# Kernel tuning notes

Measured on AMD Instinct MI355X. Metric: run time of the kernel, lower is better.

## Reference

```python
import jax, jax.numpy as jnp
import numpy as np

B, S, E, H = 4, 2048, 1024, 16
D = E // H  # head dim = 64


def setup_inputs() -> dict:
    key = jax.random.key(0)
    ks = jax.random.split(key, 5)
    s = 0.02
    return {
        "x": jax.random.normal(ks[0], (B, S, E), dtype=jnp.float32),
        "Wq": jax.random.normal(ks[1], (E, E), dtype=jnp.float32) * s,
        "Wk": jax.random.normal(ks[2], (E, E), dtype=jnp.float32) * s,
        "Wv": jax.random.normal(ks[3], (E, E), dtype=jnp.float32) * s,
        "Wo": jax.random.normal(ks[4], (E, E), dtype=jnp.float32) * s,
        "bo": jnp.zeros((E,), dtype=jnp.float32),
    }


def reference(x, Wq, Wk, Wv, Wo, bo):
    b, s, e = x.shape
    h, d = H, e // H
    # QKV projections -> [b, h, s, d]
    q = (x @ Wq).reshape(b, s, h, d).transpose(0, 2, 1, 3)
    k = (x @ Wk).reshape(b, s, h, d).transpose(0, 2, 1, 3)
    v = (x @ Wv).reshape(b, s, h, d).transpose(0, 2, 1, 3)
    # scores [b, h, s, s], causal mask with -inf, scaled softmax
    a = jnp.einsum('bhqd,bhkd->bhqk', q, k)
    causal = jnp.tril(jnp.ones((s, s), dtype=bool))  # True where allowed
    a = jnp.where(causal, a, -jnp.inf) / jnp.sqrt(jnp.asarray(d, x.dtype))
    a = jax.nn.softmax(a, axis=-1)
    # dropout p=0.0 (identity in eval)
    y = jnp.einsum('bhqk,bhkd->bhqd', a, v)
    y = y.transpose(0, 2, 1, 3).reshape(b, s, e)
    return y @ Wo + bo
```

## Files before the change

### kernel.cpp

```cpp
#include <hip/hip_runtime.h>

typedef __bf16 bf16x8 __attribute__((ext_vector_type(8)));
typedef float f32x4 __attribute__((ext_vector_type(4)));
typedef float f32x16 __attribute__((ext_vector_type(16)));
typedef unsigned short u16x8 __attribute__((ext_vector_type(8)));
typedef unsigned int u32x4 __attribute__((ext_vector_type(4)));
typedef unsigned int u32x2v __attribute__((ext_vector_type(2)));

#define S_LEN 2048
#define NHEAD 16
#define HDIM  64
#define EMB   1024

__device__ __forceinline__ ushort f2b(float v) {
  union { float f; unsigned u; } x; x.f = v;
  unsigned r = (x.u + 0x7fffu + ((x.u >> 16) & 1u)) >> 16;
  return (ushort)r;
}

__device__ __forceinline__ unsigned pk2(float lo, float hi) {
  union { float f; unsigned u; } a, b; a.f = lo; b.f = hi;
  return (b.u & 0xffff0000u) | (a.u >> 16);
}

typedef const __attribute__((address_space(1))) unsigned int* gp1_t;
typedef __attribute__((address_space(3))) unsigned int* lp3_t;
__device__ __forceinline__ void gld16(const ushort* g, const ushort* l) {
  __builtin_amdgcn_global_load_lds((gp1_t)(unsigned long long)(uintptr_t)g,
                                   (lp3_t)(unsigned int)(uintptr_t)l, 16, 0, 0);
}

__device__ __forceinline__ void barf() {
  asm volatile("" ::: "memory");
  __builtin_amdgcn_s_barrier();
  asm volatile("" ::: "memory");
}

__global__ __launch_bounds__(256) void prep_kernel(
    const float* __restrict__ x, const float* __restrict__ W0,
    const float* __restrict__ W1, const float* __restrict__ W2,
    const float* __restrict__ W3, ushort* __restrict__ xb,
    ushort* __restrict__ Wt0, ushort* __restrict__ Wt1,
    ushort* __restrict__ Wt2, ushort* __restrict__ Wt3, float scale0) {
  const int z = blockIdx.z;
  if (z == 4) {
    size_t base = ((size_t)(blockIdx.y * 32 + blockIdx.x)) * 8192 + threadIdx.x * 4;
#pragma unroll
    for (int i = 0; i < 8; ++i) {
      float4 v = *(const float4*)(x + base + i * 1024);
      ushort4 o;
      o.x = f2b(v.x); o.y = f2b(v.y); o.z = f2b(v.z); o.w = f2b(v.w);
      *(ushort4*)(xb + base + i * 1024) = o;
    }
    return;
  }
  __shared__ float t[32][33];
  const float* W = z == 0 ? W0 : (z == 1 ? W1 : (z == 2 ? W2 : W3));
  ushort* Wt = z == 0 ? Wt0 : (z == 1 ? Wt1 : (z == 2 ? Wt2 : Wt3));
  const float scale = z == 0 ? scale0 : 1.0f;
  int k0 = blockIdx.x * 32, n0 = blockIdx.y * 32;
  int c = threadIdx.x & 31, r0 = threadIdx.x >> 5;
#pragma unroll
  for (int i = 0; i < 4; ++i) {
    int r = r0 + i * 8;
    t[r][c] = W[(size_t)(k0 + r) * EMB + n0 + c];
  }
  __syncthreads();
#pragma unroll
  for (int i = 0; i < 4; ++i) {
    int r = r0 + i * 8;
    Wt[(size_t)(n0 + r) * EMB + k0 + c] = f2b(t[c][r] * scale);
  }
}

template <int EPI>
__global__ __launch_bounds__(512, 2) void gemm8_kernel(
    const ushort* __restrict__ A, const ushort* __restrict__ Bt,
    ushort* __restrict__ outQ, ushort* __restrict__ outK, ushort* __restrict__ outVt,
    float* __restrict__ outF, const float* __restrict__ bias) {
  __shared__ ushort lds8[73728];
  const int tid = threadIdx.x;
  const int wave = tid >> 6, lane = tid & 63, ln = lane & 15, quad = lane >> 4;
  const int wm = wave >> 2, wn = wave & 3;
  const long m0 = (long)blockIdx.x * 128, n0 = (long)blockIdx.y * 256;
  constexpr int K = EMB, KT = K / 64;

  const int srow = tid >> 3;
  const int scol = ((tid & 7) ^ (srow & 7)) * 8;
  const ushort* srcA = A + (m0 + srow) * (long)K + scol;
  const ushort* srcB = Bt + (n0 + srow) * (long)K + scol;

#define STG_A(t, s)                                                            \
  do {                                                                         \
    gld16(srcA + (t) * 64,               lds8 + (s) * 8192 + tid * 8);         \
    gld16(srcA + (t) * 64 + 64 * K,      lds8 + (s) * 8192 + 4096 + tid * 8);  \
  } while (0)
#define STG_B(t, s)                                                            \
  do {                                                                         \
    gld16(srcB + (t) * 64,               lds8 + 24576 + (s) * 16384 + tid * 8);         \
    gld16(srcB + (t) * 64 + 64 * K,      lds8 + 24576 + (s) * 16384 + 4096 + tid * 8);  \
    gld16(srcB + (t) * 64 + 128 * K,     lds8 + 24576 + (s) * 16384 + 8192 + tid * 8);  \
    gld16(srcB + (t) * 64 + 192 * K,     lds8 + 24576 + (s) * 16384 + 12288 + tid * 8); \
  } while (0)

  const int sw = (ln & 7) * 8;

#define RD_A(F, kk, s)                                                         \
  do {                                                                         \
    const ushort* p_ = lds8 + (s) * 8192 + (wm * 64 + ln) * 64 +               \
                       (((kk) * 32 + quad * 8) ^ sw);                          \
    F[0] = *(const bf16x8*)p_;                                                 \
    F[1] = *(const bf16x8*)(p_ + 1024);                                        \
    F[2] = *(const bf16x8*)(p_ + 2048);                                        \
    F[3] = *(const bf16x8*)(p_ + 3072);                                        \
  } while (0)
#define RD_B(F, kk, s)                                                         \
  do {                                                                         \
    const ushort* p_ = lds8 + 24576 + (s) * 16384 + (wn * 64 + ln) * 64 +      \
                       (((kk) * 32 + quad * 8) ^ sw);                          \
    F[0] = *(const bf16x8*)p_;                                                 \
    F[1] = *(const bf16x8*)(p_ + 1024);                                        \
    F[2] = *(const bf16x8*)(p_ + 2048);                                        \
    F[3] = *(const bf16x8*)(p_ + 3072);                                        \
  } while (0)

#define MM16(AF, BF)                                                           \
  do {                                                                         \
    __builtin_amdgcn_s_setprio(1);                                             \
    _Pragma("unroll") for (int mt = 0; mt < 4; ++mt)                           \
        _Pragma("unroll") for (int nt = 0; nt < 4; ++nt)                       \
            acc[mt][nt] = __builtin_amdgcn_mfma_f32_16x16x32_bf16(             \
                AF[mt], BF[nt], acc[mt][nt], 0, 0, 0);                         \
    __builtin_amdgcn_s_setprio(0);                                             \
  } while (0)

  f32x4 acc[4][4] = {};
  bf16x8 afP[4], bfP[4], afN[4], bfN[4];

  STG_A(0, 0); STG_B(0, 0);
  STG_A(1, 1); STG_B(1, 1);
  asm volatile("s_waitcnt vmcnt(6)" ::: "memory");
  barf();
  RD_A(afP, 0, 0); RD_B(bfP, 0, 0);

#define TILE_FULL(t, s, s1, s2)                                                \
  do {                                                                         \
    STG_A((t) + 2, s2);                                                        \
    RD_A(afN, 1, s); RD_B(bfN, 1, s);                                          \
    MM16(afP, bfP);                                                            \
    STG_B((t) + 2, s2);                                                        \
    asm volatile("s_waitcnt vmcnt(6) lgkmcnt(0)" ::: "memory");                \
    barf();                                                                    \
    RD_A(afP, 0, s1); RD_B(bfP, 0, s1);                                        \
    MM16(afN, bfN);                                                            \
  } while (0)

  for (int th = 0; th < 12; th += 3) {
    TILE_FULL(th, 0, 1, 2);
    TILE_FULL(th + 1, 1, 2, 0);
    TILE_FULL(th + 2, 2, 0, 1);
  }
  TILE_FULL(12, 0, 1, 2);
  TILE_FULL(13, 1, 2, 0);
  RD_A(afN, 1, 2); RD_B(bfN, 1, 2);
  MM16(afP, bfP);
  asm volatile("s_waitcnt vmcnt(0) lgkmcnt(0)" ::: "memory");
  barf();
  RD_A(afP, 0, 0); RD_B(bfP, 0, 0);
  MM16(afN, bfN);
  RD_A(afN, 1, 0); RD_B(bfN, 1, 0);
  MM16(afP, bfP);
  MM16(afN, bfN);

  if (EPI == 0) {
    const int sel = (int)(n0 >> 10);
    if (sel == 2) {
#pragma unroll
      for (int mt = 0; mt < 4; ++mt) {
        const long mbase = m0 + wm * 64 + mt * 16 + quad * 4;
        const long bb = mbase >> 11, s = mbase & 2047;
#pragma unroll
        for (int nt = 0; nt < 4; ++nt) {
          const int nn = (int)((n0 & 1023) + wn * 64 + nt * 16 + ln);
          const int h = nn >> 6, d = nn & 63;
          uint2 val;
          val.x = (unsigned)f2b(acc[mt][nt][0]) | ((unsigned)f2b(acc[mt][nt][1]) << 16);
          val.y = (unsigned)f2b(acc[mt][nt][2]) | ((unsigned)f2b(acc[mt][nt][3]) << 16);
          *(uint2*)(outVt + (((bb * NHEAD + h) * (long)HDIM + d) * S_LEN) + s) = val;
        }
      }
    } else {
      ushort* dst = sel == 0 ? outQ : outK;
#pragma unroll
      for (int mt = 0; mt < 4; ++mt) {
#pragma unroll
        for (int nt = 0; nt < 4; ++nt) {
          const int nn = (int)((n0 & 1023) + wn * 64 + nt * 16 + ln);
          const int h = nn >> 6, d = nn & 63;
#pragma unroll
          for (int r = 0; r < 4; ++r) {
            const long m = m0 + wm * 64 + mt * 16 + quad * 4 + r;
            const long bb = m >> 11, s = m & 2047;
            dst[(((bb * NHEAD + h) * S_LEN) + s) * HDIM + d] = f2b(acc[mt][nt][r]);
          }
        }
      }
    }
  } else {
#pragma unroll
    for (int mt = 0; mt < 4; ++mt) {
#pragma unroll
      for (int nt = 0; nt < 4; ++nt) {
        const long n = n0 + wn * 64 + nt * 16 + ln;
        const float bv = bias[n];
#pragma unroll
        for (int r = 0; r < 4; ++r) {
          const long m = m0 + wm * 64 + mt * 16 + quad * 4 + r;
          outF[m * (long)EMB + n] = acc[mt][nt][r] + bv;
        }
      }
    }
  }
#undef TILE_FULL
#undef MM16
#undef RD_B
#undef RD_A
#undef STG_B
#undef STG_A
}

__global__ __launch_bounds__(256, 3) void attn_kernel(const ushort* __restrict__ Q,
                                                      const ushort* __restrict__ Kg,
                                                      const ushort* __restrict__ Vt,
                                                      ushort* __restrict__ Y) {
  __shared__ alignas(16) ushort Ks[3][4096];
  __shared__ alignas(16) ushort Vs[3][4096];
  const int tid = threadIdx.x;
  const int wave = tid >> 6, lane = tid & 63;
  const int l31 = lane & 31, hi = lane >> 5;
  const int bh = blockIdx.x;
  const int qb = 15 - (int)blockIdx.y;
  const int q0 = qb * 128;
  const size_t base = (size_t)bh * S_LEN * HDIM;
  const int ntiles = 2 * qb + 2;

  const u16x8 ob = {0x3F80, 0x3F80, 0x3F80, 0x3F80, 0x3F80, 0x3F80, 0x3F80, 0x3F80};
  const bf16x8 ones = __builtin_bit_cast(bf16x8, ob);

  bf16x8 qf[4];
#pragma unroll
  for (int dsub = 0; dsub < 4; ++dsub)
    qf[dsub] = *(const bf16x8*)(Q + base + (size_t)(q0 + wave * 32 + l31) * HDIM +
                                dsub * 16 + hi * 8);

  f32x16 acc0 = {}, acc1 = {}, accl = {};

  const int srow = tid >> 3;
  const int scc  = ((tid & 7) ^ (srow & 7)) * 8;
  const ushort* KgS = Kg + base + (size_t)srow * HDIM + scc;
  const ushort* VgS = Vt + base + (size_t)srow * S_LEN + scc;

#define STAGE(t, s)                                                            \
  do {                                                                         \
    const size_t kk_ = (size_t)(t) * 64;                                       \
    gld16(KgS + kk_ * HDIM,               &Ks[s][0] + tid * 8);                \
    gld16(KgS + (kk_ + 32) * HDIM,        &Ks[s][0] + 2048 + tid * 8);         \
    gld16(VgS + kk_,                      &Vs[s][0] + tid * 8);                \
    gld16(VgS + 32 * (size_t)S_LEN + kk_, &Vs[s][0] + 2048 + tid * 8);         \
  } while (0)

  STAGE(0, 0);
  STAGE(1, 1);
  asm volatile("s_waitcnt vmcnt(4)" ::: "memory");
  barf();

  const int swL = (lane & 7) * 8;
  const int qbase = q0 + wave * 32;
  int sc = 0, sn = 1, ss = 2;

  for (int kt = 0; kt < ntiles; ++kt) {
    const int k0 = kt * 64;
    const bool do_stage = (kt + 2 < ntiles);
    if (do_stage) STAGE(kt + 2, ss);

    const ushort* Kc = &Ks[sc][0];
    const ushort* Vc = &Vs[sc][0];

    if (k0 < qbase + 32) {
      f32x16 sT0 = {}, sT1 = {};
      __builtin_amdgcn_s_setprio(1);
#pragma unroll
      for (int dsub = 0; dsub < 4; ++dsub) {
        const int c = (dsub * 16 + hi * 8) ^ swL;
        bf16x8 kf0 = *(const bf16x8*)(Kc + l31 * 64 + c);
        bf16x8 kf1 = *(const bf16x8*)(Kc + (32 + l31) * 64 + c);
        sT0 = __builtin_amdgcn_mfma_f32_32x32x16_bf16(kf0, qf[dsub], sT0, 0, 0, 0);
        sT1 = __builtin_amdgcn_mfma_f32_32x32x16_bf16(kf1, qf[dsub], sT1, 0, 0, 0);
      }
      __builtin_amdgcn_s_setprio(0);

      if (k0 + 63 > qbase) {
        const int rowq = qbase + l31;
#pragma unroll
        for (int r = 0; r < 16; ++r) {
          const int key = k0 + ((r & 3) + 8 * (r >> 2)) + 4 * hi;
          if (key > rowq) sT0[r] = -3.0e38f;
          if (key + 32 > rowq) sT1[r] = -3.0e38f;
        }
      }

      unsigned pw0[8], pw1[8];
#pragma unroll
      for (int i = 0; i < 8; ++i) {
        pw0[i] = pk2(__builtin_amdgcn_exp2f(sT0[2 * i]),
                     __builtin_amdgcn_exp2f(sT0[2 * i + 1]));
        pw1[i] = pk2(__builtin_amdgcn_exp2f(sT1[2 * i]),
                     __builtin_amdgcn_exp2f(sT1[2 * i + 1]));
      }

#define KEYBLK(PW, KSQ0)                                                       \
  do {                                                                         \
    u32x2v r02 = __builtin_amdgcn_permlane32_swap(PW[0], PW[2], false, false); \
    u32x2v r13 = __builtin_amdgcn_permlane32_swap(PW[1], PW[3], false, false); \
    u32x2v r46 = __builtin_amdgcn_permlane32_swap(PW[4], PW[6], false, false); \
    u32x2v r57 = __builtin_amdgcn_permlane32_swap(PW[5], PW[7], false, false); \
    u32x4 fwA, fwB;                                                            \
    fwA[0] = r02[0]; fwA[1] = r13[0]; fwA[2] = r02[1]; fwA[3] = r13[1];        \
    fwB[0] = r46[0]; fwB[1] = r57[0]; fwB[2] = r46[1]; fwB[3] = r57[1];        \
    bf16x8 paA = __builtin_bit_cast(bf16x8, fwA);                              \
    bf16x8 paB = __builtin_bit_cast(bf16x8, fwB);                              \
    __builtin_amdgcn_s_setprio(1);                                             \
    accl = __builtin_amdgcn_mfma_f32_32x32x16_bf16(paA, ones, accl, 0, 0, 0);  \
    accl = __builtin_amdgcn_mfma_f32_32x32x16_bf16(paB, ones, accl, 0, 0, 0);  \
    {                                                                          \
      const int vcA = (((KSQ0)) * 16 + hi * 8) ^ swL;                          \
      bf16x8 va0 = *(const bf16x8*)(Vc + l31 * 64 + vcA);                      \
      bf16x8 va1 = *(const bf16x8*)(Vc + (32 + l31) * 64 + vcA);               \
      acc0 = __builtin_amdgcn_mfma_f32_32x32x16_bf16(paA, va0, acc0, 0, 0, 0); \
      acc1 = __builtin_amdgcn_mfma_f32_32x32x16_bf16(paA, va1, acc1, 0, 0, 0); \
      const int vcB = (((KSQ0) + 1) * 16 + hi * 8) ^ swL;                      \
      bf16x8 vb0 = *(const bf16x8*)(Vc + l31 * 64 + vcB);                      \
      bf16x8 vb1 = *(const bf16x8*)(Vc + (32 + l31) * 64 + vcB);               \
      acc0 = __builtin_amdgcn_mfma_f32_32x32x16_bf16(paB, vb0, acc0, 0, 0, 0); \
      acc1 = __builtin_amdgcn_mfma_f32_32x32x16_bf16(paB, vb1, acc1, 0, 0, 0); \
    }                                                                          \
    __builtin_amdgcn_s_setprio(0);                                             \
  } while (0)

      KEYBLK(pw0, 0);
      KEYBLK(pw1, 2);
#undef KEYBLK
    }

    if (kt + 1 < ntiles) {
      if (do_stage) {
        asm volatile("s_waitcnt vmcnt(4) lgkmcnt(0)" ::: "memory");
      } else {
        asm volatile("s_waitcnt vmcnt(0) lgkmcnt(0)" ::: "memory");
      }
      barf();
    }
    const int t_ = sc; sc = sn; sn = ss; ss = t_;
  }
#undef STAGE

  const long b = bh >> 4;
  const int h = bh & 15;
#pragma unroll
  for (int r = 0; r < 16; ++r) {
    const float inv = 1.0f / accl[r];
    const int qq = q0 + wave * 32 + ((r & 3) + 8 * (r >> 2)) + 4 * hi;
    ushort* yp = Y + (((b * S_LEN + qq) * NHEAD) + h) * HDIM;
    yp[l31]      = f2b(acc0[r] * inv);
    yp[32 + l31] = f2b(acc1[r] * inv);
  }
}

extern "C" void kernel_launch(void* const* d_in, const int* in_sizes, int n_in,
                              void* d_out, int out_size, void* d_ws, size_t ws_size,
                              hipStream_t stream) {
  const float* x  = (const float*)d_in[0];
  const float* Wq = (const float*)d_in[1];
  const float* Wk = (const float*)d_in[2];
  const float* Wv = (const float*)d_in[3];
  const float* Wo = (const float*)d_in[4];
  const float* bo = (const float*)d_in[5];
  float* out = (float*)d_out;

  const size_t XE = (size_t)8192 * EMB;
  ushort* ws    = (ushort*)d_ws;
  ushort* xb    = ws;
  ushort* Wtqkv = xb + XE;
  ushort* Wto   = Wtqkv + 3 * 1048576;
  ushort* Qb    = Wto + 1048576;
  ushort* Kb    = Qb + XE;
  ushort* Vtb   = Kb + XE;
  ushort* Yb    = xb;

  const float SCALE_Q = 1.4426950408889634f / 8.0f;

  prep_kernel<<<dim3(32, 32, 5), 256, 0, stream>>>(
      x, Wq, Wk, Wv, Wo, xb, Wtqkv, Wtqkv + 1048576, Wtqkv + 2097152, Wto, SCALE_Q);

  gemm8_kernel<0><<<dim3(64, 12), 512, 0, stream>>>(xb, Wtqkv, Qb, Kb, Vtb,
                                                    nullptr, nullptr);
  attn_kernel<<<dim3(64, 16), 256, 0, stream>>>(Qb, Kb, Vtb, Yb);
  gemm8_kernel<1><<<dim3(64, 4), 512, 0, stream>>>(Yb, Wto, nullptr, nullptr,
                                                   nullptr, out, bo);
}
```

Before: 229.7 us.

## Use 256x256 tile GEMM kernel with double buffering for QKV projection

Adds a dedicated QKV projection kernel with 256x256 output tiles, where each wave computes a 128x64 subtile (8x4 MFMAs) from a two-stage LDS double buffer. The old 128x256 triple-buffered path is kept only for the output projection. Larger tiles raise arithmetic intensity and cut global reloads of A and B. In exchange the grid shrinks to 384 blocks, which may underfill the GPU. The kernel also uses more accumulator registers and 128KB of LDS, which can limit occupancy and latency hiding.

```diff
diff --git a/kernel.cpp b/kernel.cpp
--- a/kernel.cpp
+++ b/kernel.cpp
@@ -73,10 +73,125 @@
   }
 }
 
+__global__ __launch_bounds__(512, 2) void gemm256_kernel(
+    const ushort* __restrict__ A, const ushort* __restrict__ Bt,
+    ushort* __restrict__ outQ, ushort* __restrict__ outK,
+    ushort* __restrict__ outVt) {
+  __shared__ ushort lds2[65536];
+  const int tid = threadIdx.x;
+  const int wave = tid >> 6, lane = tid & 63, ln = lane & 15, quad = lane >> 4;
+  const int wm = wave >> 2, wn = wave & 3;
+  const long m0 = (long)blockIdx.x * 256, n0 = (long)blockIdx.y * 256;
+  constexpr int K = EMB, KT = K / 64;
+
+  const int srow = tid >> 3;
+  const int scol = ((tid & 7) ^ (srow & 7)) * 8;
+  const ushort* srcA = A + (m0 + srow) * (long)K + scol;
+  const ushort* srcB = Bt + (n0 + srow) * (long)K + scol;
+
+#define STG_A(t, b)                                                            \
+  do {                                                                         \
+    _Pragma("unroll") for (int ld = 0; ld < 4; ++ld)                           \
+        gld16(srcA + (t) * 64 + ld * 64 * K,                                   \
+              lds2 + (b) * 16384 + ld * 4096 + tid * 8);                       \
+  } while (0)
+#define STG_B(t, b)                                                            \
+  do {                                                                         \
+    _Pragma("unroll") for (int ld = 0; ld < 4; ++ld)                           \
+        gld16(srcB + (t) * 64 + ld * 64 * K,                                   \
+              lds2 + 32768 + (b) * 16384 + ld * 4096 + tid * 8);               \
+  } while (0)
+
+  const int sw = (ln & 7) * 8;
+
+#define RD_A8(F, kk, b)                                                        \
+  do {                                                                         \
+    const ushort* p_ = lds2 + (b) * 16384 + (wm * 128 + ln) * 64 +             \
+                       (((kk) * 32 + quad * 8) ^ sw);                          \
+    _Pragma("unroll") for (int m_ = 0; m_ < 8; ++m_)                           \
+        F[m_] = *(const bf16x8*)(p_ + m_ * 1024);                              \
+  } while (0)
+#define RD_B4(F, kk, b)                                                        \
+  do {                                                                         \
+    const ushort* p_ = lds2 + 32768 + (b) * 16384 + (wn * 64 + ln) * 64 +      \
+                       (((kk) * 32 + quad * 8) ^ sw);                          \
+    _Pragma("unroll") for (int n_ = 0; n_ < 4; ++n_)                           \
+        F[n_] = *(const bf16x8*)(p_ + n_ * 1024);                              \
+  } while (0)
+
+#define MM32(AF, BF)                                                           \
+  do {                                                                         \
+    __builtin_amdgcn_s_setprio(1);                                             \
+    _Pragma("unroll") for (int mt = 0; mt < 8; ++mt)                           \
+        _Pragma("unroll") for (int nt = 0; nt < 4; ++nt)                       \
+            acc[mt][nt] = __builtin_amdgcn_mfma_f32_16x16x32_bf16(             \
+                AF[mt], BF[nt], acc[mt][nt], 0, 0, 0);                         \
+    __builtin_amdgcn_s_setprio(0);                                             \
+  } while (0)
+
+  f32x4 acc[8][4] = {};
+  bf16x8 afP[8], bfP[4], afN[8], bfN[4];
+
+  STG_A(0, 0); STG_B(0, 0);
+  asm volatile("s_waitcnt vmcnt(0)" ::: "memory");
+  barf();
+
+  for (int kt = 0; kt < KT; ++kt) {
+    const int bb = kt & 1;
+    if (kt + 1 < KT) { STG_A(kt + 1, bb ^ 1); STG_B(kt + 1, bb ^ 1); }
+    RD_A8(afP, 0, bb); RD_B4(bfP, 0, bb);
+    MM32(afP, bfP);
+    RD_A8(afN, 1, bb); RD_B4(bfN, 1, bb);
+    MM32(afN, bfN);
+    if (kt + 1 < KT) {
+      asm volatile("s_waitcnt vmcnt(0) lgkmcnt(0)" ::: "memory");
+      barf();
+    }
+  }
+
+  const int sel = (int)(n0 >> 10);
+  if (sel == 2) {
+#pragma unroll
+    for (int mt = 0; mt < 8; ++mt) {
+      const long mbase = m0 + wm * 128 + mt * 16 + quad * 4;
+      const long bb2 = mbase >> 11, s = mbase & 2047;
+#pragma unroll
+      for (int nt = 0; nt < 4; ++nt) {
+        const int nn = (int)((n0 & 1023) + wn * 64 + nt * 16 + ln);
+        const int h = nn >> 6, d = nn & 63;
+        uint2 val;
+        val.x = (unsigned)f2b(acc[mt][nt][0]) | ((unsigned)f2b(acc[mt][nt][1]) << 16);
+        val.y = (unsigned)f2b(acc[mt][nt][2]) | ((unsigned)f2b(acc[mt][nt][3]) << 16);
+        *(uint2*)(outVt + (((bb2 * NHEAD + h) * (long)HDIM + d) * S_LEN) + s) = val;
+      }
+    }
+  } else {
+    ushort* dst = sel == 0 ? outQ : outK;
+#pragma unroll
+    for (int mt = 0; mt < 8; ++mt) {
+#pragma unroll
+      for (int nt = 0; nt < 4; ++nt) {
+        const int nn = (int)((n0 & 1023) + wn * 64 + nt * 16 + ln);
+        const int h = nn >> 6, d = nn & 63;
+#pragma unroll
+        for (int r = 0; r < 4; ++r) {
+          const long m = m0 + wm * 128 + mt * 16 + quad * 4 + r;
+          const long bb2 = m >> 11, s = m & 2047;
+          dst[(((bb2 * NHEAD + h) * S_LEN) + s) * HDIM + d] = f2b(acc[mt][nt][r]);
+        }
+      }
+    }
+  }
+#undef MM32
+#undef RD_B4
+#undef RD_A8
+#undef STG_B
+#undef STG_A
+}
+
 template <int EPI>
 __global__ __launch_bounds__(512, 2) void gemm8_kernel(
     const ushort* __restrict__ A, const ushort* __restrict__ Bt,
-    ushort* __restrict__ outQ, ushort* __restrict__ outK, ushort* __restrict__ outVt,
     float* __restrict__ outF, const float* __restrict__ bias) {
   __shared__ ushort lds8[73728];
   const int tid = threadIdx.x;
@@ -172,52 +287,16 @@
   MM16(afP, bfP);
   MM16(afN, bfN);
 
-  if (EPI == 0) {
-    const int sel = (int)(n0 >> 10);
-    if (sel == 2) {
-#pragma unroll
-      for (int mt = 0; mt < 4; ++mt) {
-        const long mbase = m0 + wm * 64 + mt * 16 + quad * 4;
-        const long bb = mbase >> 11, s = mbase & 2047;
-#pragma unroll
-        for (int nt = 0; nt < 4; ++nt) {
-          const int nn = (int)((n0 & 1023) + wn * 64 + nt * 16 + ln);
-          const int h = nn >> 6, d = nn & 63;
-          uint2 val;
-          val.x = (unsigned)f2b(acc[mt][nt][0]) | ((unsigned)f2b(acc[mt][nt][1]) << 16);
-          val.y = (unsigned)f2b(acc[mt][nt][2]) | ((unsigned)f2b(acc[mt][nt][3]) << 16);
-          *(uint2*)(outVt + (((bb * NHEAD + h) * (long)HDIM + d) * S_LEN) + s) = val;
-        }
-      }
-    } else {
-      ushort* dst = sel == 0 ? outQ : outK;
-#pragma unroll
-      for (int mt = 0; mt < 4; ++mt) {
-#pragma unroll
-        for (int nt = 0; nt < 4; ++nt) {
-          const int nn = (int)((n0 & 1023) + wn * 64 + nt * 16 + ln);
-          const int h = nn >> 6, d = nn & 63;
-#pragma unroll
-          for (int r = 0; r < 4; ++r) {
-            const long m = m0 + wm * 64 + mt * 16 + quad * 4 + r;
-            const long bb = m >> 11, s = m & 2047;
-            dst[(((bb * NHEAD + h) * S_LEN) + s) * HDIM + d] = f2b(acc[mt][nt][r]);
-          }
-        }
-      }
-    }
-  } else {
-#pragma unroll
-    for (int mt = 0; mt < 4; ++mt) {
-#pragma unroll
-      for (int nt = 0; nt < 4; ++nt) {
-        const long n = n0 + wn * 64 + nt * 16 + ln;
-        const float bv = bias[n];
-#pragma unroll
-        for (int r = 0; r < 4; ++r) {
-          const long m = m0 + wm * 64 + mt * 16 + quad * 4 + r;
-          outF[m * (long)EMB + n] = acc[mt][nt][r] + bv;
-        }
+#pragma unroll
+  for (int mt = 0; mt < 4; ++mt) {
+#pragma unroll
+    for (int nt = 0; nt < 4; ++nt) {
+      const long n = n0 + wn * 64 + nt * 16 + ln;
+      const float bv = bias[n];
+#pragma unroll
+      for (int r = 0; r < 4; ++r) {
+        const long m = m0 + wm * 64 + mt * 16 + quad * 4 + r;
+        outF[m * (long)EMB + n] = acc[mt][nt][r] + bv;
       }
     }
   }
@@ -402,9 +481,7 @@
   prep_kernel<<<dim3(32, 32, 5), 256, 0, stream>>>(
       x, Wq, Wk, Wv, Wo, xb, Wtqkv, Wtqkv + 1048576, Wtqkv + 2097152, Wto, SCALE_Q);
 
-  gemm8_kernel<0><<<dim3(64, 12), 512, 0, stream>>>(xb, Wtqkv, Qb, Kb, Vtb,
-                                                    nullptr, nullptr);
+  gemm256_kernel<<<dim3(32, 12), 512, 0, stream>>>(xb, Wtqkv, Qb, Kb, Vtb);
   attn_kernel<<<dim3(64, 16), 256, 0, stream>>>(Qb, Kb, Vtb, Yb);
-  gemm8_kernel<1><<<dim3(64, 4), 512, 0, stream>>>(Yb, Wto, nullptr, nullptr,
-                                                   nullptr, out, bo);
-}
+  gemm8_kernel<1><<<dim3(64, 4), 512, 0, stream>>>(Yb, Wto, out, bo);
+}
```

New measurement: 232.1 us. No clear change (+1.0%).
